# Optimization experiments

Measured on AMD Instinct MI355X. Metric: run time of the kernel, lower is better.

Reference implementation:

```python
import jax, jax.numpy as jnp
import numpy as np

EPS = 1e-6

def _avgpool(x, k):
    # AvgPool2d(kernel_size=k, stride=k) for divisible H, W
    B, C, H, W = x.shape
    return x.reshape(B, C, H // k, k, W // k, k).mean(axis=(3, 5))

def setup_inputs() -> dict:
    key = jax.random.key(0)
    ks = jax.random.split(key, 5)
    B, C, H, W, kern = 32, 128, 32, 32, 2
    shp = (B, C, H, W)
    return {
        "mu_a_": jax.random.normal(ks[0], shp, dtype=jnp.float32),
        "logvar_a_": jax.random.normal(ks[1], shp, dtype=jnp.float32),
        "mu_b_": jax.random.normal(ks[2], shp, dtype=jnp.float32),
        "logvar_b_": jax.random.normal(ks[3], shp, dtype=jnp.float32),
        "eps": jax.random.normal(ks[4], (B, C, H // kern, W // kern), dtype=jnp.float32),
        "kern": kern,
    }

def _log_mean_density(z, mu, var):
    # z: [B,C,h,w] (one MC sample per batch row i); mu/var: [B,C,h,w]
    # pairwise unnormalized Gaussian density ratio, mean over the mixture (j) axis
    d = jnp.exp(-(z[:, None] - mu[None]) ** 2 / (2.0 * var[None])) / jnp.sqrt(var[None])  # [B,B,C,h,w]
    return jnp.log(jnp.mean(d, axis=1) + EPS)  # [B,C,h,w]

def reference(mu_a_, logvar_a_, mu_b_, logvar_b_, eps, kern):
    k = int(kern)
    mu_a = _avgpool(mu_a_, k)
    mu_b = _avgpool(mu_b_, k)
    var_a = _avgpool(jnp.exp(logvar_a_), k) / (k * k)
    var_b = _avgpool(jnp.exp(logvar_b_), k) / (k * k)
    z = mu_a + jnp.sqrt(var_a) * eps  # reparameterized MC samples, one per row
    term = _log_mean_density(z, mu_a, var_a) - _log_mean_density(z, mu_b, var_b)  # [B,C,h,w]
    # torch loop adds each per-i term (shape [C,h,w]) broadcast into a [B,C,h,w]
    # accumulator, then sums -> equals B * sum_i,c,h,w term
    B = mu_a.shape[0]
    return jnp.asarray(B, term.dtype) * jnp.sum(term)
```

## Files before the change

### kernel.cpp

```cpp
#include <hip/hip_runtime.h>


#define GKL_EPS 1e-6f
#define LOG2E 1.44269504f

__global__ __launch_bounds__(256) void gkl_main(
    const float* __restrict__ muA, const float* __restrict__ lvA,
    const float* __restrict__ muB, const float* __restrict__ lvB,
    const float* __restrict__ eps, double* __restrict__ ws)
{
    __shared__ float sh[3628];

    const int bid = blockIdx.x;
    const int c   = bid >> 4;
    const int h   = bid & 15;
    const int t   = threadIdx.x;
    const int w   = t & 15;
    const int b0  = t >> 4;

    #pragma unroll
    for (int rep = 0; rep < 2; ++rep) {
        const int b = b0 + rep*16;
        const int base = ((b*128 + c)*32 + 2*h)*32 + 2*w;
        const int qw = ((b >> 2)*3)*64 + w*4 + (b & 3);

        float2 m0 = *(const float2*)(muA + base);
        float2 m1 = *(const float2*)(muA + base + 32);
        float2 l0 = *(const float2*)(lvA + base);
        float2 l1 = *(const float2*)(lvA + base + 32);
        float mu  = (m0.x + m0.y + m1.x + m1.y) * 0.25f;
        float var = (__builtin_amdgcn_exp2f(l0.x*LOG2E) + __builtin_amdgcn_exp2f(l0.y*LOG2E)
                   + __builtin_amdgcn_exp2f(l1.x*LOG2E) + __builtin_amdgcn_exp2f(l1.y*LOG2E)) * 0.0625f;
        float c2  = -0.72134752f * __builtin_amdgcn_rcpf(var);
        float ls  = fmaf(-0.5f, __builtin_amdgcn_logf(var), -0.2356196f);
        sh[qw]       = mu;
        sh[qw + 64]  = c2;
        sh[qw + 128] = ls;
        float ev = eps[((b*128 + c)*16 + h)*16 + w];
        sh[3080 + b*17 + w] = fmaf(__builtin_amdgcn_sqrtf(var), ev, mu);

        float2 n0 = *(const float2*)(muB + base);
        float2 n1 = *(const float2*)(muB + base + 32);
        float2 k0 = *(const float2*)(lvB + base);
        float2 k1 = *(const float2*)(lvB + base + 32);
        float mub  = (n0.x + n0.y + n1.x + n1.y) * 0.25f;
        float varb = (__builtin_amdgcn_exp2f(k0.x*LOG2E) + __builtin_amdgcn_exp2f(k0.y*LOG2E)
                    + __builtin_amdgcn_exp2f(k1.x*LOG2E) + __builtin_amdgcn_exp2f(k1.y*LOG2E)) * 0.0625f;
        float c2b  = -0.72134752f * __builtin_amdgcn_rcpf(varb);
        float lsb  = fmaf(-0.5f, __builtin_amdgcn_logf(varb), -0.2356196f);
        sh[1540 + qw]       = mub;
        sh[1540 + qw + 64]  = c2b;
        sh[1540 + qw + 128] = lsb;
    }
    __syncthreads();

    const int lane = t & 63;
    const int wv   = t >> 6;
    const int i    = lane & 31;
    const int side = lane >> 5;
    const float* __restrict__ Qb = sh + side*1540;
    const float* __restrict__ zp = sh + 3080;
    float* __restrict__ wsum     = sh + 3624;

    float tot = 0.f;
    #pragma unroll
    for (int q = 0; q < 4; ++q) {
        const int p  = wv*4 + q;
        const float zi = zp[i*17 + p];
        const float* base = Qb + p*4;
        float accA = 0.f, accB = 0.f;
        #pragma unroll
        for (int g = 0; g < 8; ++g) {
            float4 m  = *(const float4*)(base + g*192);
            float4 cc = *(const float4*)(base + g*192 + 64);
            float4 ll = *(const float4*)(base + g*192 + 128);
            float d0 = zi - m.x, d1 = zi - m.y, d2 = zi - m.z, d3 = zi - m.w;
            accA += __builtin_amdgcn_exp2f(fmaf(d0*d0, cc.x, ll.x));
            accB += __builtin_amdgcn_exp2f(fmaf(d1*d1, cc.y, ll.y));
            accA += __builtin_amdgcn_exp2f(fmaf(d2*d2, cc.z, ll.z));
            accB += __builtin_amdgcn_exp2f(fmaf(d3*d3, cc.w, ll.w));
        }
        float lg = __builtin_amdgcn_logf(fmaf(accA + accB, 0.036794063f, GKL_EPS));
        tot += side ? -lg : lg;
    }

    #pragma unroll
    for (int o = 32; o; o >>= 1) tot += __shfl_xor(tot, o, 64);
    if (lane == 0) wsum[wv] = tot;
    __syncthreads();
    if (t == 0)
        ws[bid] = (double)wsum[0] + (double)wsum[1] + (double)wsum[2] + (double)wsum[3];
}

__global__ __launch_bounds__(256) void gkl_final(
    const double* __restrict__ ws, float* __restrict__ out)
{
    __shared__ double part[4];
    const int t = threadIdx.x;
    double s = 0.0;
    for (int k = t; k < 2048; k += 256) s += ws[k];
    #pragma unroll
    for (int o = 32; o; o >>= 1) s += __shfl_xor(s, o, 64);
    if ((t & 63) == 0) part[t >> 6] = s;
    __syncthreads();
    if (t == 0) out[0] = (float)(0.69314718055994531 * 32.0 *
                                 (part[0] + part[1] + part[2] + part[3]));
}

extern "C" void kernel_launch(void* const* d_in, const int* in_sizes, int n_in,
                              void* d_out, int out_size, void* d_ws, size_t ws_size,
                              hipStream_t stream) {
    const float* muA = (const float*)d_in[0];
    const float* lvA = (const float*)d_in[1];
    const float* muB = (const float*)d_in[2];
    const float* lvB = (const float*)d_in[3];
    const float* ep  = (const float*)d_in[4];
    double* ws = (double*)d_ws;
    float* out = (float*)d_out;

    gkl_main<<<2048, 256, 0, stream>>>(muA, lvA, muB, lvB, ep, ws);
    gkl_final<<<1, 256, 0, stream>>>(ws, out);
}
```

Before: 111.4 us.

## Reparameterize Gaussian term as scaled difference to cut LDS operands

Precomputes a per-component scale s = c/sqrt(var) and s*mu so each density term becomes exp2(-(z*s - s*mu)^2) weighted by s. This drops the per-element log/rcp precompute and reduces shared-memory operands per term from three to two, with an interleaved padded layout and two samples processed per loop. The exp count is unchanged, and rounding behaviour shifts slightly.

```diff
diff --git a/kernel.cpp b/kernel.cpp
--- a/kernel.cpp
+++ b/kernel.cpp
@@ -9,7 +9,7 @@
     const float* __restrict__ muB, const float* __restrict__ lvB,
     const float* __restrict__ eps, double* __restrict__ ws)
 {
-    __shared__ float sh[3628];
+    __shared__ float sh[2732];
 
     const int bid = blockIdx.x;
     const int c   = bid >> 4;
@@ -22,7 +22,6 @@
     for (int rep = 0; rep < 2; ++rep) {
         const int b = b0 + rep*16;
         const int base = ((b*128 + c)*32 + 2*h)*32 + 2*w;
-        const int qw = ((b >> 2)*3)*64 + w*4 + (b & 3);
 
         float2 m0 = *(const float2*)(muA + base);
         float2 m1 = *(const float2*)(muA + base + 32);
@@ -31,13 +30,11 @@
         float mu  = (m0.x + m0.y + m1.x + m1.y) * 0.25f;
         float var = (__builtin_amdgcn_exp2f(l0.x*LOG2E) + __builtin_amdgcn_exp2f(l0.y*LOG2E)
                    + __builtin_amdgcn_exp2f(l1.x*LOG2E) + __builtin_amdgcn_exp2f(l1.y*LOG2E)) * 0.0625f;
-        float c2  = -0.72134752f * __builtin_amdgcn_rcpf(var);
-        float ls  = fmaf(-0.5f, __builtin_amdgcn_logf(var), -0.2356196f);
-        sh[qw]       = mu;
-        sh[qw + 64]  = c2;
-        sh[qw + 128] = ls;
+        float rs  = __builtin_amdgcn_rsqf(var);
+        float s   = 0.84932185f * rs;
+        *(float2*)(sh + w*68 + 2*b) = make_float2(s, s*mu);
         float ev = eps[((b*128 + c)*16 + h)*16 + w];
-        sh[3080 + b*17 + w] = fmaf(__builtin_amdgcn_sqrtf(var), ev, mu);
+        sh[2184 + b*17 + w] = fmaf(var*rs, ev, mu);
 
         float2 n0 = *(const float2*)(muB + base);
         float2 n1 = *(const float2*)(muB + base + 32);
@@ -46,11 +43,9 @@
         float mub  = (n0.x + n0.y + n1.x + n1.y) * 0.25f;
         float varb = (__builtin_amdgcn_exp2f(k0.x*LOG2E) + __builtin_amdgcn_exp2f(k0.y*LOG2E)
                     + __builtin_amdgcn_exp2f(k1.x*LOG2E) + __builtin_amdgcn_exp2f(k1.y*LOG2E)) * 0.0625f;
-        float c2b  = -0.72134752f * __builtin_amdgcn_rcpf(varb);
-        float lsb  = fmaf(-0.5f, __builtin_amdgcn_logf(varb), -0.2356196f);
-        sh[1540 + qw]       = mub;
-        sh[1540 + qw + 64]  = c2b;
-        sh[1540 + qw + 128] = lsb;
+        float rsb  = __builtin_amdgcn_rsqf(varb);
+        float sb   = 0.84932185f * rsb;
+        *(float2*)(sh + 1092 + w*68 + 2*b) = make_float2(sb, sb*mub);
     }
     __syncthreads();
 
@@ -58,31 +53,36 @@
     const int wv   = t >> 6;
     const int i    = lane & 31;
     const int side = lane >> 5;
-    const float* __restrict__ Qb = sh + side*1540;
-    const float* __restrict__ zp = sh + 3080;
-    float* __restrict__ wsum     = sh + 3624;
+    const float* __restrict__ Qb = sh + side*1092;
+    const float* __restrict__ zp = sh + 2184;
+    float* __restrict__ wsum     = sh + 2728;
 
-    float tot = 0.f;
+    float lg = 0.f;
     #pragma unroll
-    for (int q = 0; q < 4; ++q) {
-        const int p  = wv*4 + q;
-        const float zi = zp[i*17 + p];
-        const float* base = Qb + p*4;
-        float accA = 0.f, accB = 0.f;
+    for (int q = 0; q < 2; ++q) {
+        const int p0 = wv*4 + 2*q, p1 = p0 + 1;
+        const float z0 = zp[i*17 + p0];
+        const float z1 = zp[i*17 + p1];
+        const float* qp0 = Qb + p0*68;
+        const float* qp1 = Qb + p1*68;
+        float acc0 = 0.f, acc1 = 0.f;
         #pragma unroll
-        for (int g = 0; g < 8; ++g) {
-            float4 m  = *(const float4*)(base + g*192);
-            float4 cc = *(const float4*)(base + g*192 + 64);
-            float4 ll = *(const float4*)(base + g*192 + 128);
-            float d0 = zi - m.x, d1 = zi - m.y, d2 = zi - m.z, d3 = zi - m.w;
-            accA += __builtin_amdgcn_exp2f(fmaf(d0*d0, cc.x, ll.x));
-            accB += __builtin_amdgcn_exp2f(fmaf(d1*d1, cc.y, ll.y));
-            accA += __builtin_amdgcn_exp2f(fmaf(d2*d2, cc.z, ll.z));
-            accB += __builtin_amdgcn_exp2f(fmaf(d3*d3, cc.w, ll.w));
+        for (int k = 0; k < 16; ++k) {
+            float4 f = *(const float4*)(qp0 + 4*k);
+            float4 g = *(const float4*)(qp1 + 4*k);
+            float e0 = fmaf(z0, f.x, -f.y);
+            acc0 = fmaf(f.x, __builtin_amdgcn_exp2f(-(e0*e0)), acc0);
+            float e1 = fmaf(z0, f.z, -f.w);
+            acc0 = fmaf(f.z, __builtin_amdgcn_exp2f(-(e1*e1)), acc0);
+            float e2 = fmaf(z1, g.x, -g.y);
+            acc1 = fmaf(g.x, __builtin_amdgcn_exp2f(-(e2*e2)), acc1);
+            float e3 = fmaf(z1, g.z, -g.w);
+            acc1 = fmaf(g.z, __builtin_amdgcn_exp2f(-(e3*e3)), acc1);
         }
-        float lg = __builtin_amdgcn_logf(fmaf(accA + accB, 0.036794063f, GKL_EPS));
-        tot += side ? -lg : lg;
+        lg += __builtin_amdgcn_logf(fmaf(acc0, 0.036794063f, GKL_EPS))
+            + __builtin_amdgcn_logf(fmaf(acc1, 0.036794063f, GKL_EPS));
     }
+    float tot = side ? -lg : lg;
 
     #pragma unroll
     for (int o = 32; o; o >>= 1) tot += __shfl_xor(tot, o, 64);
```

New measurement: 110.6 us. Within noise of the previous version (-0.7%).
